# Kernel tuning notes

Hardware: AMD Instinct MI355X
Metric: run time of the kernel (lower is better)

## Reference

```python
import jax, jax.numpy as jnp
import numpy as np
import math

B, L, T, IN, H, DEPTH, HEADS = 4096, 1, 64, 16, 128, 3, 2
HD = H // HEADS
EPS = 1e-5


def layer_norm(x, g, b):
    u = jnp.mean(x, axis=-1, keepdims=True)
    s = jnp.mean((x - u) ** 2, axis=-1, keepdims=True)
    return g * (x - u) / jnp.sqrt(s + EPS) + b


def mlp(x, W, b, g, beta):
    return jax.nn.relu(layer_norm(x @ W + b, g, beta))


def attention(h, amask, Wq, bq, Wk, bk, Wv, bv):
    N, Tn, _ = h.shape
    def heads(x):
        return x.reshape(N, Tn, HEADS, HD).transpose(0, 2, 1, 3)
    q = heads(h @ Wq + bq)
    k = heads(h @ Wk + bk)
    v = heads(h @ Wv + bv)
    scores = jnp.einsum('nhqd,nhkd->nhqk', q, k) / math.sqrt(HD)
    scores = scores + (1.0 - amask[:, None]) * -10000.0
    probs = jax.nn.softmax(scores, axis=-1)
    ctx = jnp.einsum('nhqk,nhkd->nhqd', probs, v)
    return ctx.transpose(0, 2, 1, 3).reshape(N, Tn, H)


def setup_inputs() -> dict:
    key = jax.random.key(0)
    ks = jax.random.split(key, 8)
    feat = jax.random.normal(ks[0], (B, L, T, IN), jnp.float32)
    seq_lens = jax.random.randint(ks[1], (B, L), 1, T + 1)
    pos = jnp.arange(T)
    # repo convention: 0 = valid node, 1 = padded; prefix-valid layout
    masks = (pos[None, None, :] >= seq_lens[..., None]).astype(jnp.float32)[..., None]
    s = 0.02
    W_emb = jax.random.normal(ks[2], (IN, H), jnp.float32) * s
    W_enc = jax.random.normal(ks[3], (H, H), jnp.float32) * s
    Wq = jax.random.normal(ks[4], (DEPTH, H, H), jnp.float32) * s
    Wk = jax.random.normal(ks[5], (DEPTH, H, H), jnp.float32) * s
    Wv = jax.random.normal(ks[6], (DEPTH, H, H), jnp.float32) * s
    return dict(
        lane_nodes_feat=feat, masks=masks,
        W_emb=W_emb, b_emb=jnp.zeros((H,)), g_emb=jnp.ones((H,)), beta_emb=jnp.zeros((H,)),
        W_enc=W_enc, b_enc=jnp.zeros((H,)), g_enc=jnp.ones((H,)), beta_enc=jnp.zeros((H,)),
        Wq=Wq, bq=jnp.zeros((DEPTH, H)), Wk=Wk, bk=jnp.zeros((DEPTH, H)), Wv=Wv, bv=jnp.zeros((DEPTH, H)),
        ln_g=jnp.ones((DEPTH, H)), ln_b=jnp.zeros((DEPTH, H)),
    )


def reference(lane_nodes_feat, masks, W_emb, b_emb, g_emb, beta_emb, W_enc, b_enc,
              g_enc, beta_enc, Wq, bq, Wk, bk, Wv, bv, ln_g, ln_b):
    emb = mlp(lane_nodes_feat, W_emb, b_emb, g_emb, beta_emb)   # [B,L,T,H]
    emb = mlp(emb, W_enc, b_enc, g_enc, beta_enc)
    # every (b,l) lane has >=1 valid node by construction, so masked_select == reshape
    hs = emb.reshape(B * L, T, H)
    seq_lens = jnp.sum(1.0 - masks[:, :, :, 0], axis=-1).reshape(B * L)  # [N]
    pos = jnp.arange(T)
    valid = pos[None, :] < seq_lens[:, None]                              # [N,T]
    amask = (valid[:, :, None] & valid[:, None, :]).astype(hs.dtype)      # [N,T,T]
    for d in range(DEPTH):
        temp = hs
        hs = attention(hs, amask, Wq[d], bq[d], Wk[d], bk[d], Wv[d], bv[d])
        hs = jax.nn.relu(hs) + temp
        hs = layer_norm(hs, ln_g[d], ln_b[d])
    hs = jnp.max(hs, axis=1)                                              # [N,H]
    return hs.reshape(B, L, H)
```

## Files before the change

### kernel.cpp

```cpp
#include <hip/hip_runtime.h>

typedef unsigned short u16;
typedef unsigned int u32;
typedef __attribute__((ext_vector_type(8))) short short8;
typedef __attribute__((ext_vector_type(4))) float floatx4;

#define EPSV 1e-5f
#define WS_ELEMS 167936

__device__ __forceinline__ float b2f(u16 u){
  union { float f; u32 i; } c; c.i = ((u32)u) << 16; return c.f;
}
__device__ __forceinline__ u16 f2b(float f){
  union { float f; u32 i; } c; c.f = f;
  u32 r = c.i + 0x7FFFu + ((c.i >> 16) & 1u);
  return (u16)(r >> 16);
}
__device__ __forceinline__ u16 f2bc(float f){
  union { float f; u32 i; } c; c.f = f;
  return (u16)((c.i + 0x8000u) >> 16);
}
__device__ __forceinline__ float ldf(const void* p, int i, bool isf){
  return isf ? ((const float*)p)[i] : b2f(((const u16*)p)[i]);
}
__device__ __forceinline__ bool detect_f32(const void* g_emb){
  return *(const u32*)g_emb == 0x3F800000u;
}
__device__ __forceinline__ void dma16(const u16* g, u16* l){
  __builtin_amdgcn_global_load_lds((const __attribute__((address_space(1))) u32*)(g),
                                   (__attribute__((address_space(3))) u32*)(l), 16, 0, 0);
}
__device__ __forceinline__ void dma_slab(const u16* g, u16* dst, int wave, int lane){
  #pragma unroll
  for (int i = 0; i < 4; i++){
    int c = (wave << 2) + i;
    dma16(g + (c << 9) + (lane << 3), dst + (c << 9));
  }
}

__global__ void prep_kernel(const void* W_emb, const void* W_enc,
                            const void* Wq, const void* Wk, const void* Wv,
                            const void* g_emb, u16* ws){
  bool isf = detect_f32(g_emb);
  int e = blockIdx.x * 256 + threadIdx.x;
  if (e >= WS_ELEMS) return;
  float v;
  if (e < 4096){
    int half = e >> 11, r = e & 2047;
    int nt = r >> 9, q = (r >> 3) & 63, j = r & 7;
    int col = half*64 + nt*16 + (q & 15);
    int k = (q >> 4)*8 + j;
    v = (k < 16) ? ldf(W_emb, k*128 + col, isf) : 0.0f;
  } else if (e < 20480){
    int i = e - 4096;
    int half = i >> 13, r = i & 8191;
    int chunk = r >> 9, q = (r >> 3) & 63, j = r & 7;
    int ks = chunk >> 2, nt = chunk & 3;
    int col = half*64 + nt*16 + (q & 15);
    int k = ks*32 + (q >> 4)*8 + j;
    v = ldf(W_enc, k*128 + col, isf);
  } else {
    int i = e - 20480;
    int slab = i >> 13, r = i & 8191;
    int dh = slab / 3, which = slab - dh*3;
    int d = dh >> 1, h = dh & 1;
    int chunk = r >> 9, q = (r >> 3) & 63, j = r & 7;
    int ks = chunk >> 2, nt = chunk & 3;
    int col = h*64 + nt*16 + (q & 15);
    int k = ks*32 + (q >> 4)*8 + j;
    const void* W = (which == 0) ? Wv : (which == 1) ? Wk : Wq;
    v = ldf(W, d*16384 + k*128 + col, isf);
  }
  ws[e] = f2b(v);
}

__device__ __forceinline__ short8 frg(const u16* p, int chunk, int lane){
  return *(const short8*)(p + (chunk << 9) + (lane << 3));
}
__device__ __forceinline__ int wfoff(int wave, int nt, int lq, int lc){
  return ((((nt >> 1) << 2) + wave) << 9)
       + ((((((nt << 1) + (lc >> 3)) & 3) << 4) + (lq << 2)) << 3) + (lc & 7);
}
__device__ __forceinline__ int qfoff(int wave, int nt, int lq, int lc){
  return (wave << 10) + ((nt >> 1) << 9)
       + ((((((nt << 1) + (lc >> 3)) & 3) << 4) + (lq << 2)) << 3) + (lc & 7);
}

__device__ __forceinline__ void gemmW(const u16* sh, const u16* slab, int wave, int lane, floatx4* acc){
  #pragma unroll
  for (int ks = 0; ks < 4; ks++){
    short8 a = frg(sh, ks*4 + wave, lane);
    #pragma unroll
    for (int nt = 0; nt < 4; nt++)
      acc[nt] = __builtin_amdgcn_mfma_f32_16x16x32_bf16(a, frg(slab, ks*4 + nt, lane), acc[nt], 0, 0, 0);
  }
}
__device__ __forceinline__ void gemmWT(const u16* sh, const u16* slab, int wave, int lane, floatx4* acc){
  #pragma unroll
  for (int ks = 0; ks < 4; ks++){
    short8 a = frg(slab, ks*4 + wave, lane);
    #pragma unroll
    for (int nt = 0; nt < 4; nt++)
      acc[nt] = __builtin_amdgcn_mfma_f32_16x16x32_bf16(a, frg(sh, ks*4 + nt, lane), acc[nt], 0, 0, 0);
  }
}
__device__ __forceinline__ void gemm64(const u16* areg, const u16* b, int wave, int lane, floatx4* acc){
  #pragma unroll
  for (int ks = 0; ks < 2; ks++){
    short8 a = *(const short8*)(areg + (wave << 10) + (ks << 9) + (lane << 3));
    #pragma unroll
    for (int nt = 0; nt < 4; nt++)
      acc[nt] = __builtin_amdgcn_mfma_f32_16x16x32_bf16(a, frg(b, ks*4 + nt, lane), acc[nt], 0, 0, 0);
  }
}

__device__ __forceinline__ void red_sum2(float* s1, float* s2){
  #pragma unroll
  for (int m = 1; m < 16; m <<= 1){
    #pragma unroll
    for (int r = 0; r < 4; r++){
      s1[r] += __shfl_xor(s1[r], m, 64);
      s2[r] += __shfl_xor(s2[r], m, 64);
    }
  }
}

__device__ __forceinline__ void ln_mlp(floatx4* acc, const void* bias, const void* g,
    const void* bet, bool isf, int wave, int lq, int lc, u16* sh){
  float x[8][4], s1[4] = {0,0,0,0}, s2[4] = {0,0,0,0};
  #pragma unroll
  for (int nt = 0; nt < 8; nt++){
    float bb = ldf(bias, nt*16 + lc, isf);
    #pragma unroll
    for (int r = 0; r < 4; r++){
      float v = acc[nt][r] + bb;
      x[nt][r] = v; s1[r] += v; s2[r] += v*v;
    }
  }
  red_sum2(s1, s2);
  float mean[4], rstd[4];
  #pragma unroll
  for (int r = 0; r < 4; r++){
    mean[r] = s1[r] * (1.0f/128.0f);
    rstd[r] = rsqrtf(s2[r]*(1.0f/128.0f) - mean[r]*mean[r] + EPSV);
  }
  #pragma unroll
  for (int nt = 0; nt < 8; nt++){
    float gg = ldf(g, nt*16 + lc, isf), bb = ldf(bet, nt*16 + lc, isf);
    int o = wfoff(wave, nt, lq, lc);
    #pragma unroll
    for (int r = 0; r < 4; r++){
      float y = (x[nt][r] - mean[r]) * rstd[r] * gg + bb;
      sh[o + 8*r] = f2bc(fmaxf(y, 0.0f));
    }
  }
}

__device__ __forceinline__ void ln_attn(floatx4* ctx, const u16* cb,
                                        int wave, int lq, int lc, u16* sh){
  float x[8][4], s1[4] = {0,0,0,0}, s2[4] = {0,0,0,0};
  #pragma unroll
  for (int nt = 0; nt < 8; nt++){
    int o = wfoff(wave, nt, lq, lc);
    #pragma unroll
    for (int r = 0; r < 4; r++){
      float v = fmaxf(ctx[nt][r], 0.0f) + b2f(sh[o + 8*r]);
      x[nt][r] = v; s1[r] += v; s2[r] += v*v;
    }
  }
  red_sum2(s1, s2);
  float mean[4], rstd[4];
  #pragma unroll
  for (int r = 0; r < 4; r++){
    mean[r] = s1[r] * (1.0f/128.0f);
    rstd[r] = rsqrtf(s2[r]*(1.0f/128.0f) - mean[r]*mean[r] + EPSV);
  }
  #pragma unroll
  for (int nt = 0; nt < 8; nt++){
    float gg = b2f(cb[384 + nt*16 + lc]), bb = b2f(cb[512 + nt*16 + lc]);
    int o = wfoff(wave, nt, lq, lc);
    #pragma unroll
    for (int r = 0; r < 4; r++){
      float y = (x[nt][r] - mean[r]) * rstd[r] * gg + bb;
      sh[o + 8*r] = f2bc(y);
    }
  }
}

__global__ __launch_bounds__(256, 3)
void fused_kernel(const void* feat, const void* masks,
                  const void* b_emb, const void* g_emb, const void* be_emb,
                  const void* b_enc, const void* g_enc, const void* be_enc,
                  const void* bq, const void* bk, const void* bv,
                  const void* ln_g, const void* ln_b,
                  const u16* ws, void* out){
  __shared__ __align__(16) u16 s_h[8192];
  __shared__ __align__(16) u16 s_w[8192];
  __shared__ __align__(16) u16 s_k[4096];
  __shared__ __align__(16) u16 s_v[4096];
  __shared__ u16 s_c[1920];
  __shared__ float s_valid[64];

  int tid = threadIdx.x;
  int wave = tid >> 6, lane = tid & 63, lq = lane >> 4, lc = lane & 15;
  int n = blockIdx.x;
  bool isf = detect_f32(g_emb);
  const floatx4 z4 = {0.0f, 0.0f, 0.0f, 0.0f};

  dma16(ws + ((wave*2 + 0) << 9) + (lane << 3), s_w + ((wave*2 + 0) << 9));
  dma16(ws + ((wave*2 + 1) << 9) + (lane << 3), s_w + ((wave*2 + 1) << 9));

  if (!isf){
    const u16* fp = (const u16*)feat + n*1024;
    if (tid < 128){
      int t = tid >> 1, half = tid & 1;
      uint4 v = *(const uint4*)(fp + t*16 + half*8);
      *(uint4*)(s_h + ((t >> 4) << 9) + (((half << 4) + (t & 15)) << 3)) = v;
    } else {
      int t = (tid - 128) >> 1, half = 2 + ((tid - 128) & 1);
      uint4 z; z.x = z.y = z.z = z.w = 0;
      *(uint4*)(s_h + ((t >> 4) << 9) + (((half << 4) + (t & 15)) << 3)) = z;
    }
  } else {
    for (int i = tid; i < 2048; i += 256){
      int t = i >> 5, k = i & 31;
      float v = (k < 16) ? ((const float*)feat)[n*1024 + t*16 + k] : 0.0f;
      s_h[((t >> 4) << 9) + ((((k >> 3) << 4) + (t & 15)) << 3) + (k & 7)] = f2b(v);
    }
  }
  for (int i = tid; i < 1920; i += 256){
    int blk = i >> 7, off = i & 127;
    int d = blk / 5, wh = blk - d*5;
    const void* src = (wh == 0) ? bq : (wh == 1) ? bk : (wh == 2) ? bv : (wh == 3) ? ln_g : ln_b;
    s_c[i] = isf ? f2b(((const float*)src)[d*128 + off]) : ((const u16*)src)[d*128 + off];
  }
  if (tid < 64) s_valid[tid] = (ldf(masks, n*64 + tid, isf) == 0.0f) ? 1.0f : 0.0f;
  __syncthreads();

  floatx4 acc[8];
  #pragma unroll
  for (int i = 0; i < 8; i++) acc[i] = z4;
  {
    short8 a = frg(s_h, wave, lane);
    #pragma unroll
    for (int nt = 0; nt < 4; nt++){
      acc[nt]     = __builtin_amdgcn_mfma_f32_16x16x32_bf16(a, frg(s_w, nt,     lane), acc[nt],     0,0,0);
      acc[4 + nt] = __builtin_amdgcn_mfma_f32_16x16x32_bf16(a, frg(s_w, 4 + nt, lane), acc[4 + nt], 0,0,0);
    }
  }
  __syncthreads();
  dma_slab(ws + 4096, s_w, wave, lane);
  ln_mlp(acc, b_emb, g_emb, be_emb, isf, wave, lq, lc, s_h);
  __syncthreads();

  #pragma unroll
  for (int i = 0; i < 8; i++) acc[i] = z4;
  gemmW(s_h, s_w, wave, lane, acc);
  __syncthreads();
  dma_slab(ws + 12288, s_w, wave, lane);
  __syncthreads();
  gemmW(s_h, s_w, wave, lane, acc + 4);
  __syncthreads();
  dma_slab(ws + 20480, s_w, wave, lane);
  ln_mlp(acc, b_enc, g_enc, be_enc, isf, wave, lq, lc, s_h);
  __syncthreads();

  int sb = 20480;
  for (int d = 0; d < 3; d++){
    const u16* cb = s_c + d*640;
    floatx4 ctx[8];
    #pragma unroll
    for (int i = 0; i < 8; i++) ctx[i] = z4;

    for (int h = 0; h < 2; h++){
      floatx4 pa[4];
      #pragma unroll
      for (int i = 0; i < 4; i++) pa[i] = z4;
      gemmWT(s_h, s_w, wave, lane, pa);
      __syncthreads();
      dma_slab(ws + sb + 8192, s_w, wave, lane);
      {
        float bb4[4];
        #pragma unroll
        for (int r = 0; r < 4; r++) bb4[r] = b2f(cb[256 + h*64 + wave*16 + (lq << 2) + r]);
        #pragma unroll
        for (int nt = 0; nt < 4; nt++){
          int o = wfoff(wave, nt, lq, lc);
          #pragma unroll
          for (int r = 0; r < 4; r++) s_v[o + 8*r] = f2bc(pa[nt][r] + bb4[r]);
        }
      }
      __syncthreads();
      #pragma unroll
      for (int i = 0; i < 4; i++) pa[i] = z4;
      gemmW(s_h, s_w, wave, lane, pa);
      __syncthreads();
      dma_slab(ws + sb + 16384, s_w, wave, lane);
      {
        #pragma unroll
        for (int nt = 0; nt < 4; nt++){
          float bb = b2f(cb[128 + h*64 + nt*16 + lc]);
          int o = wfoff(wave, nt, lq, lc);
          #pragma unroll
          for (int r = 0; r < 4; r++) s_k[o + 8*r] = f2bc(pa[nt][r] + bb);
        }
      }
      __syncthreads();
      #pragma unroll
      for (int i = 0; i < 4; i++) pa[i] = z4;
      gemmW(s_h, s_w, wave, lane, pa);
      __syncthreads();
      {
        #pragma unroll
        for (int nt = 0; nt < 4; nt++){
          float bb = b2f(cb[h*64 + nt*16 + lc]);
          int o = qfoff(wave, nt, lq, lc);
          #pragma unroll
          for (int r = 0; r < 4; r++) s_w[o + 8*r] = f2bc(pa[nt][r] + bb);
        }
      }
      #pragma unroll
      for (int i = 0; i < 4; i++) pa[i] = z4;
      gemm64(s_w, s_k, wave, lane, pa);

      float rv[4], cv[4];
      #pragma unroll
      for (int r = 0; r < 4; r++) rv[r] = s_valid[wave*16 + (lq << 2) + r];
      #pragma unroll
      for (int nt = 0; nt < 4; nt++) cv[nt] = s_valid[nt*16 + lc];

      float p[4][4];
      #pragma unroll
      for (int nt = 0; nt < 4; nt++)
        #pragma unroll
        for (int r = 0; r < 4; r++)
          p[nt][r] = pa[nt][r]*0.125f - 10000.0f*(1.0f - rv[r]*cv[nt]);

      float mx[4];
      #pragma unroll
      for (int r = 0; r < 4; r++)
        mx[r] = fmaxf(fmaxf(p[0][r], p[1][r]), fmaxf(p[2][r], p[3][r]));
      #pragma unroll
      for (int m = 1; m < 16; m <<= 1)
        #pragma unroll
        for (int r = 0; r < 4; r++) mx[r] = fmaxf(mx[r], __shfl_xor(mx[r], m, 64));

      float sm[4] = {0,0,0,0};
      #pragma unroll
      for (int nt = 0; nt < 4; nt++)
        #pragma unroll
        for (int r = 0; r < 4; r++){ p[nt][r] = __expf(p[nt][r] - mx[r]); sm[r] += p[nt][r]; }
      #pragma unroll
      for (int m = 1; m < 16; m <<= 1)
        #pragma unroll
        for (int r = 0; r < 4; r++) sm[r] += __shfl_xor(sm[r], m, 64);

      float inv[4];
      #pragma unroll
      for (int r = 0; r < 4; r++) inv[r] = 1.0f / sm[r];

      #pragma unroll
      for (int nt = 0; nt < 4; nt++){
        int o = qfoff(wave, nt, lq, lc);
        #pragma unroll
        for (int r = 0; r < 4; r++) s_w[o + 8*r] = f2bc(p[nt][r] * inv[r]);
      }
      gemm64(s_w, s_v, wave, lane, ctx + h*4);
      __syncthreads();
      sb += 24576;
      if (!(d == 2 && h == 1)) dma_slab(ws + sb, s_w, wave, lane);
      if (h == 1) ln_attn(ctx, cb, wave, lq, lc, s_h);
      __syncthreads();
    }
  }

  if (tid < 128){
    int col = tid;
    float mxv = -1e30f;
    #pragma unroll 4
    for (int t = 0; t < 64; t++)
      mxv = fmaxf(mxv, b2f(s_h[((((col >> 5) << 2) + (t >> 4)) << 9)
                               + (((((col >> 3) & 3) << 4) + (t & 15)) << 3) + (col & 7)]));
    if (isf) ((float*)out)[n*128 + col] = mxv;
    else     ((u16*)out)[n*128 + col] = f2b(mxv);
  }
}

extern "C" void kernel_launch(void* const* d_in, const int* in_sizes, int n_in,
                              void* d_out, int out_size, void* d_ws, size_t ws_size,
                              hipStream_t stream){
  const void* feat   = d_in[0];
  const void* masks  = d_in[1];
  const void* W_emb  = d_in[2];
  const void* b_emb  = d_in[3];
  const void* g_emb  = d_in[4];
  const void* be_emb = d_in[5];
  const void* W_enc  = d_in[6];
  const void* b_enc  = d_in[7];
  const void* g_enc  = d_in[8];
  const void* be_enc = d_in[9];
  const void* Wq     = d_in[10];
  const void* bq     = d_in[11];
  const void* Wk     = d_in[12];
  const void* bk     = d_in[13];
  const void* Wv     = d_in[14];
  const void* bv     = d_in[15];
  const void* ln_g   = d_in[16];
  const void* ln_b   = d_in[17];
  u16* ws = (u16*)d_ws;

  hipLaunchKernelGGL(prep_kernel, dim3((WS_ELEMS + 255)/256), dim3(256), 0, stream,
                     W_emb, W_enc, Wq, Wk, Wv, g_emb, ws);
  hipLaunchKernelGGL(fused_kernel, dim3(4096), dim3(256), 0, stream,
                     feat, masks, b_emb, g_emb, be_emb, b_enc, g_enc, be_enc,
                     bq, bk, bv, ln_g, ln_b, ws, d_out);
}
```

Baseline: 389.9 us.

## Swizzle LDS fragment layout, 2x2 wave tiling for QKV GEMMs, keep residual in registers

Introduces an XOR-swizzled fragment layout for LDS tiles and prepacked weights to reduce bank conflicts on fragment reads and writes. The per-head Q/K/V projections switch from a 1x4 per-wave tiling to a 2x2 wave tiling, so each wave loads fewer distinct fragments per k-step. The residual activations are kept in fp32 registers (xres) rather than re-read from LDS as bf16, which removes LDS reads and rounding of the residual at the cost of 32 extra registers per thread, a risk at 3 blocks per CU.

```diff
diff --git a/kernel.cpp b/kernel.cpp
--- a/kernel.cpp
+++ b/kernel.cpp
@@ -36,6 +36,15 @@
     int c = (wave << 2) + i;
     dma16(g + (c << 9) + (lane << 3), dst + (c << 9));
   }
+}
+__device__ __forceinline__ int swz(int lane){
+  return (lane & ~3) | ((lane ^ (lane >> 2)) & 3);
+}
+__device__ __forceinline__ int fragoff(int chunk, int quad, int m, int j){
+  return (chunk << 9) + ((((quad << 4) | (m & 12) | ((m ^ (m >> 2)) & 3))) << 3) + j;
+}
+__device__ __forceinline__ short8 frg(const u16* p, int chunk, int swl){
+  return *(const short8*)(p + (chunk << 9) + (swl << 3));
 }
 
 __global__ void prep_kernel(const void* W_emb, const void* W_enc,
@@ -47,17 +56,19 @@
   float v;
   if (e < 4096){
     int half = e >> 11, r = e & 2047;
-    int nt = r >> 9, q = (r >> 3) & 63, j = r & 7;
-    int col = half*64 + nt*16 + (q & 15);
-    int k = (q >> 4)*8 + j;
+    int q = (r >> 3) & 63, j = r & 7;
+    int ql = (q & ~3) | ((q ^ (q >> 2)) & 3);
+    int col = half*64 + ((r >> 9) << 4) + (ql & 15);
+    int k = (ql >> 4)*8 + j;
     v = (k < 16) ? ldf(W_emb, k*128 + col, isf) : 0.0f;
   } else if (e < 20480){
     int i = e - 4096;
     int half = i >> 13, r = i & 8191;
     int chunk = r >> 9, q = (r >> 3) & 63, j = r & 7;
+    int ql = (q & ~3) | ((q ^ (q >> 2)) & 3);
     int ks = chunk >> 2, nt = chunk & 3;
-    int col = half*64 + nt*16 + (q & 15);
-    int k = ks*32 + (q >> 4)*8 + j;
+    int col = half*64 + nt*16 + (ql & 15);
+    int k = ks*32 + (ql >> 4)*8 + j;
     v = ldf(W_enc, k*128 + col, isf);
   } else {
     int i = e - 20480;
@@ -65,52 +76,38 @@
     int dh = slab / 3, which = slab - dh*3;
     int d = dh >> 1, h = dh & 1;
     int chunk = r >> 9, q = (r >> 3) & 63, j = r & 7;
+    int ql = (q & ~3) | ((q ^ (q >> 2)) & 3);
     int ks = chunk >> 2, nt = chunk & 3;
-    int col = h*64 + nt*16 + (q & 15);
-    int k = ks*32 + (q >> 4)*8 + j;
+    int col = h*64 + nt*16 + (ql & 15);
+    int k = ks*32 + (ql >> 4)*8 + j;
     const void* W = (which == 0) ? Wv : (which == 1) ? Wk : Wq;
     v = ldf(W, d*16384 + k*128 + col, isf);
   }
   ws[e] = f2b(v);
 }
 
-__device__ __forceinline__ short8 frg(const u16* p, int chunk, int lane){
-  return *(const short8*)(p + (chunk << 9) + (lane << 3));
-}
-__device__ __forceinline__ int wfoff(int wave, int nt, int lq, int lc){
-  return ((((nt >> 1) << 2) + wave) << 9)
-       + ((((((nt << 1) + (lc >> 3)) & 3) << 4) + (lq << 2)) << 3) + (lc & 7);
-}
-__device__ __forceinline__ int qfoff(int wave, int nt, int lq, int lc){
-  return (wave << 10) + ((nt >> 1) << 9)
-       + ((((((nt << 1) + (lc >> 3)) & 3) << 4) + (lq << 2)) << 3) + (lc & 7);
-}
-
-__device__ __forceinline__ void gemmW(const u16* sh, const u16* slab, int wave, int lane, floatx4* acc){
+#define MFMA(a,b,c) __builtin_amdgcn_mfma_f32_16x16x32_bf16((a),(b),(c),0,0,0)
+
+__device__ __forceinline__ void gemmW(const u16* sh, const u16* slab, int wave, int swl, floatx4* acc){
   #pragma unroll
   for (int ks = 0; ks < 4; ks++){
-    short8 a = frg(sh, ks*4 + wave, lane);
+    short8 a = frg(sh, ks*4 + wave, swl);
     #pragma unroll
     for (int nt = 0; nt < 4; nt++)
-      acc[nt] = __builtin_amdgcn_mfma_f32_16x16x32_bf16(a, frg(slab, ks*4 + nt, lane), acc[nt], 0, 0, 0);
-  }
-}
-__device__ __forceinline__ void gemmWT(const u16* sh, const u16* slab, int wave, int lane, floatx4* acc){
+      acc[nt] = MFMA(a, frg(slab, ks*4 + nt, swl), acc[nt]);
+  }
+}
+__device__ __forceinline__ void gemm2x2(const u16* A, const u16* B, int ra, int cb_, int swl, floatx4* acc){
   #pragma unroll
   for (int ks = 0; ks < 4; ks++){
-    short8 a = frg(slab, ks*4 + wave, lane);
-    #pragma unroll
-    for (int nt = 0; nt < 4; nt++)
-      acc[nt] = __builtin_amdgcn_mfma_f32_16x16x32_bf16(a, frg(sh, ks*4 + nt, lane), acc[nt], 0, 0, 0);
-  }
-}
-__device__ __forceinline__ void gemm64(const u16* areg, const u16* b, int wave, int lane, floatx4* acc){
-  #pragma unroll
-  for (int ks = 0; ks < 2; ks++){
-    short8 a = *(const short8*)(areg + (wave << 10) + (ks << 9) + (lane << 3));
-    #pragma unroll
-    for (int nt = 0; nt < 4; nt++)
-      acc[nt] = __builtin_amdgcn_mfma_f32_16x16x32_bf16(a, frg(b, ks*4 + nt, lane), acc[nt], 0, 0, 0);
+    short8 a0 = frg(A, ks*4 + ra,     swl);
+    short8 a1 = frg(A, ks*4 + ra + 1, swl);
+    short8 b0 = frg(B, ks*4 + cb_,     swl);
+    short8 b1 = frg(B, ks*4 + cb_ + 1, swl);
+    acc[0] = MFMA(a0, b0, acc[0]);
+    acc[1] = MFMA(a0, b1, acc[1]);
+    acc[2] = MFMA(a1, b0, acc[2]);
+    acc[3] = MFMA(a1, b1, acc[3]);
   }
 }
 
@@ -125,16 +122,46 @@
   }
 }
 
+__device__ __forceinline__ void pwrite_col(floatx4* a4, u16* dst, const u16* bias,
+    int wr, int wc, int lq, int lc){
+  #pragma unroll
+  for (int tc = 0; tc < 2; tc++){
+    float bb = b2f(bias[wc*32 + tc*16 + lc]);
+    #pragma unroll
+    for (int tr = 0; tr < 2; tr++){
+      #pragma unroll
+      for (int r = 0; r < 4; r++)
+        dst[fragoff(wc*4 + wr*2 + tr, tc*2 + (lc >> 3), lq*4 + r, lc & 7)]
+          = f2bc(a4[tr*2+tc][r] + bb);
+    }
+  }
+}
+__device__ __forceinline__ void pwrite_row(floatx4* a4, u16* dst, const u16* bias,
+    int wr, int wc, int lq, int lc){
+  #pragma unroll
+  for (int tr = 0; tr < 2; tr++){
+    float bb[4];
+    #pragma unroll
+    for (int r = 0; r < 4; r++) bb[r] = b2f(bias[wr*32 + tr*16 + lq*4 + r]);
+    #pragma unroll
+    for (int tc = 0; tc < 2; tc++)
+      #pragma unroll
+      for (int r = 0; r < 4; r++)
+        dst[fragoff(wc*4 + wr*2 + tr, tc*2 + (lc >> 3), lq*4 + r, lc & 7)]
+          = f2bc(a4[tr*2+tc][r] + bb[r]);
+  }
+}
+
 __device__ __forceinline__ void ln_mlp(floatx4* acc, const void* bias, const void* g,
-    const void* bet, bool isf, int wave, int lq, int lc, u16* sh){
-  float x[8][4], s1[4] = {0,0,0,0}, s2[4] = {0,0,0,0};
+    const void* bet, bool isf, float xres[8][4], int wave, int lq, int lc, u16* sh){
+  float s1[4] = {0,0,0,0}, s2[4] = {0,0,0,0};
   #pragma unroll
   for (int nt = 0; nt < 8; nt++){
     float bb = ldf(bias, nt*16 + lc, isf);
     #pragma unroll
     for (int r = 0; r < 4; r++){
       float v = acc[nt][r] + bb;
-      x[nt][r] = v; s1[r] += v; s2[r] += v*v;
+      xres[nt][r] = v; s1[r] += v; s2[r] += v*v;
     }
   }
   red_sum2(s1, s2);
@@ -147,27 +174,25 @@
   #pragma unroll
   for (int nt = 0; nt < 8; nt++){
     float gg = ldf(g, nt*16 + lc, isf), bb = ldf(bet, nt*16 + lc, isf);
-    int o = wfoff(wave, nt, lq, lc);
     #pragma unroll
     for (int r = 0; r < 4; r++){
-      float y = (x[nt][r] - mean[r]) * rstd[r] * gg + bb;
-      sh[o + 8*r] = f2bc(fmaxf(y, 0.0f));
-    }
-  }
-}
-
-__device__ __forceinline__ void ln_attn(floatx4* ctx, const u16* cb,
+      float y = fmaxf((xres[nt][r] - mean[r]) * rstd[r] * gg + bb, 0.0f);
+      xres[nt][r] = y;
+      sh[fragoff((nt >> 1)*4 + wave, ((nt & 1) << 1) + (lc >> 3), lq*4 + r, lc & 7)] = f2bc(y);
+    }
+  }
+}
+
+__device__ __forceinline__ void ln_attn(floatx4* ctx, float xres[8][4], const u16* cb,
                                         int wave, int lq, int lc, u16* sh){
-  float x[8][4], s1[4] = {0,0,0,0}, s2[4] = {0,0,0,0};
-  #pragma unroll
-  for (int nt = 0; nt < 8; nt++){
-    int o = wfoff(wave, nt, lq, lc);
+  float s1[4] = {0,0,0,0}, s2[4] = {0,0,0,0};
+  #pragma unroll
+  for (int nt = 0; nt < 8; nt++)
     #pragma unroll
     for (int r = 0; r < 4; r++){
-      float v = fmaxf(ctx[nt][r], 0.0f) + b2f(sh[o + 8*r]);
-      x[nt][r] = v; s1[r] += v; s2[r] += v*v;
-    }
-  }
+      float v = fmaxf(ctx[nt][r], 0.0f) + xres[nt][r];
+      xres[nt][r] = v; s1[r] += v; s2[r] += v*v;
+    }
   red_sum2(s1, s2);
   float mean[4], rstd[4];
   #pragma unroll
@@ -178,11 +203,11 @@
   #pragma unroll
   for (int nt = 0; nt < 8; nt++){
     float gg = b2f(cb[384 + nt*16 + lc]), bb = b2f(cb[512 + nt*16 + lc]);
-    int o = wfoff(wave, nt, lq, lc);
     #pragma unroll
     for (int r = 0; r < 4; r++){
-      float y = (x[nt][r] - mean[r]) * rstd[r] * gg + bb;
-      sh[o + 8*r] = f2bc(y);
+      float y = (xres[nt][r] - mean[r]) * rstd[r] * gg + bb;
+      xres[nt][r] = y;
+      sh[fragoff((nt >> 1)*4 + wave, ((nt & 1) << 1) + (lc >> 3), lq*4 + r, lc & 7)] = f2bc(y);
     }
   }
 }
@@ -203,6 +228,8 @@
 
   int tid = threadIdx.x;
   int wave = tid >> 6, lane = tid & 63, lq = lane >> 4, lc = lane & 15;
+  int wr = wave >> 1, wc = wave & 1;
+  int swl = swz(lane);
   int n = blockIdx.x;
   bool isf = detect_f32(g_emb);
   const floatx4 z4 = {0.0f, 0.0f, 0.0f, 0.0f};
@@ -215,17 +242,17 @@
     if (tid < 128){
       int t = tid >> 1, half = tid & 1;
       uint4 v = *(const uint4*)(fp + t*16 + half*8);
-      *(uint4*)(s_h + ((t >> 4) << 9) + (((half << 4) + (t & 15)) << 3)) = v;
+      *(uint4*)(s_h + fragoff(t >> 4, half, t & 15, 0)) = v;
     } else {
       int t = (tid - 128) >> 1, half = 2 + ((tid - 128) & 1);
       uint4 z; z.x = z.y = z.z = z.w = 0;
-      *(uint4*)(s_h + ((t >> 4) << 9) + (((half << 4) + (t & 15)) << 3)) = z;
+      *(uint4*)(s_h + fragoff(t >> 4, half, t & 15, 0)) = z;
     }
   } else {
     for (int i = tid; i < 2048; i += 256){
       int t = i >> 5, k = i & 31;
       float v = (k < 16) ? ((const float*)feat)[n*1024 + t*16 + k] : 0.0f;
-      s_h[((t >> 4) << 9) + ((((k >> 3) << 4) + (t & 15)) << 3) + (k & 7)] = f2b(v);
+      s_h[fragoff(t >> 4, k >> 3, t & 15, k & 7)] = f2b(v);
     }
   }
   for (int i = tid; i < 1920; i += 256){
@@ -237,32 +264,33 @@
   if (tid < 64) s_valid[tid] = (ldf(masks, n*64 + tid, isf) == 0.0f) ? 1.0f : 0.0f;
   __syncthreads();
 
+  float xres[8][4];
   floatx4 acc[8];
   #pragma unroll
   for (int i = 0; i < 8; i++) acc[i] = z4;
   {
-    short8 a = frg(s_h, wave, lane);
+    short8 a = frg(s_h, wave, swl);
     #pragma unroll
     for (int nt = 0; nt < 4; nt++){
-      acc[nt]     = __builtin_amdgcn_mfma_f32_16x16x32_bf16(a, frg(s_w, nt,     lane), acc[nt],     0,0,0);
-      acc[4 + nt] = __builtin_amdgcn_mfma_f32_16x16x32_bf16(a, frg(s_w, 4 + nt, lane), acc[4 + nt], 0,0,0);
+      acc[nt]     = MFMA(a, frg(s_w, nt,     swl), acc[nt]);
+      acc[4 + nt] = MFMA(a, frg(s_w, 4 + nt, swl), acc[4 + nt]);
     }
   }
   __syncthreads();
   dma_slab(ws + 4096, s_w, wave, lane);
-  ln_mlp(acc, b_emb, g_emb, be_emb, isf, wave, lq, lc, s_h);
+  ln_mlp(acc, b_emb, g_emb, be_emb, isf, xres, wave, lq, lc, s_h);
   __syncthreads();
 
   #pragma unroll
   for (int i = 0; i < 8; i++) acc[i] = z4;
-  gemmW(s_h, s_w, wave, lane, acc);
+  gemmW(s_h, s_w, wave, swl, acc);
   __syncthreads();
   dma_slab(ws + 12288, s_w, wave, lane);
   __syncthreads();
-  gemmW(s_h, s_w, wave, lane, acc + 4);
+  gemmW(s_h, s_w, wave, swl, acc + 4);
   __syncthreads();
   dma_slab(ws + 20480, s_w, wave, lane);
-  ln_mlp(acc, b_enc, g_enc, be_enc, isf, wave, lq, lc, s_h);
+  ln_mlp(acc, b_enc, g_enc, be_enc, isf, xres, wave, lq, lc, s_h);
   __syncthreads();
 
   int sb = 20480;
@@ -276,53 +304,33 @@
       floatx4 pa[4];
       #pragma unroll
       for (int i = 0; i < 4; i++) pa[i] = z4;
-      gemmWT(s_h, s_w, wave, lane, pa);
+      gemm2x2(s_w, s_h, wr*2, wc*2, swl, pa);
       __syncthreads();
       dma_slab(ws + sb + 8192, s_w, wave, lane);
-      {
-        float bb4[4];
-        #pragma unroll
-        for (int r = 0; r < 4; r++) bb4[r] = b2f(cb[256 + h*64 + wave*16 + (lq << 2) + r]);
-        #pragma unroll
-        for (int nt = 0; nt < 4; nt++){
-          int o = wfoff(wave, nt, lq, lc);
-          #pragma unroll
-          for (int r = 0; r < 4; r++) s_v[o + 8*r] = f2bc(pa[nt][r] + bb4[r]);
-        }
+      pwrite_row(pa, s_v, cb + 256 + h*64, wr, wc, lq, lc);
+      __syncthreads();
+      #pragma unroll
+      for (int i = 0; i < 4; i++) pa[i] = z4;
+      gemm2x2(s_h, s_w, wr*2, wc*2, swl, pa);
+      __syncthreads();
+      dma_slab(ws + sb + 16384, s_w, wave, lane);
+      pwrite_col(pa, s_k, cb + 128 + h*64, wr, wc, lq, lc);
+      __syncthreads();
+      #pragma unroll
+      for (int i = 0; i < 4; i++) pa[i] = z4;
+      gemm2x2(s_h, s_w, wr*2, wc*2, swl, pa);
+      __syncthreads();
+      pwrite_col(pa, s_w, cb + h*64, wr, wc, lq, lc);
+      __syncthreads();
+      #pragma unroll
+      for (int i = 0; i < 4; i++) pa[i] = z4;
+      #pragma unroll
+      for (int ks = 0; ks < 2; ks++){
+        short8 a = frg(s_w, ks*4 + wave, swl);
+        #pragma unroll
+        for (int nt = 0; nt < 4; nt++)
+          pa[nt] = MFMA(a, frg(s_k, ks*4 + nt, swl), pa[nt]);
       }
-      __syncthreads();
-      #pragma unroll
-      for (int i = 0; i < 4; i++) pa[i] = z4;
-      gemmW(s_h, s_w, wave, lane, pa);
-      __syncthreads();
-      dma_slab(ws + sb + 16384, s_w, wave, lane);
-      {
-        #pragma unroll
-        for (int nt = 0; nt < 4; nt++){
-          float bb = b2f(cb[128 + h*64 + nt*16 + lc]);
-          int o = wfoff(wave, nt, lq, lc);
-          #pragma unroll
-          for (int r = 0; r < 4; r++) s_k[o + 8*r] = f2bc(pa[nt][r] + bb);
-        }
-      }
-      __syncthreads();
-      #pragma unroll
-      for (int i = 0; i < 4; i++) pa[i] = z4;
-      gemmW(s_h, s_w, wave, lane, pa);
-      __syncthreads();
-      {
-        #pragma unroll
-        for (int nt = 0; nt < 4; nt++){
-          float bb = b2f(cb[h*64 + nt*16 + lc]);
-          int o = qfoff(wave, nt, lq, lc);
-          #pragma unroll
-          for (int r = 0; r < 4; r++) s_w[o + 8*r] = f2bc(pa[nt][r] + bb);
-        }
-      }
-      #pragma unroll
-      for (int i = 0; i < 4; i++) pa[i] = z4;
-      gemm64(s_w, s_k, wave, lane, pa);
-
       float rv[4], cv[4];
       #pragma unroll
       for (int r = 0; r < 4; r++) rv[r] = s_valid[wave*16 + (lq << 2) + r];
@@ -360,16 +368,22 @@
       for (int r = 0; r < 4; r++) inv[r] = 1.0f / sm[r];
 
       #pragma unroll
-      for (int nt = 0; nt < 4; nt++){
-        int o = qfoff(wave, nt, lq, lc);
-        #pragma unroll
-        for (int r = 0; r < 4; r++) s_w[o + 8*r] = f2bc(p[nt][r] * inv[r]);
+      for (int nt = 0; nt < 4; nt++)
+        #pragma unroll
+        for (int r = 0; r < 4; r++)
+          s_w[fragoff(8 + 2*wave + (nt >> 1), ((nt & 1) << 1) + (lc >> 3), lq*4 + r, lc & 7)]
+            = f2bc(p[nt][r] * inv[r]);
+      #pragma unroll
+      for (int ks = 0; ks < 2; ks++){
+        short8 a = frg(s_w, 8 + 2*wave + ks, swl);
+        #pragma unroll
+        for (int nt = 0; nt < 4; nt++)
+          ctx[h*4 + nt] = MFMA(a, frg(s_v, ks*4 + nt, swl), ctx[h*4 + nt]);
       }
-      gemm64(s_w, s_v, wave, lane, ctx + h*4);
       __syncthreads();
       sb += 24576;
       if (!(d == 2 && h == 1)) dma_slab(ws + sb, s_w, wave, lane);
-      if (h == 1) ln_attn(ctx, cb, wave, lq, lc, s_h);
+      if (h == 1) ln_attn(ctx, xres, cb, wave, lq, lc, s_h);
       __syncthreads();
     }
   }
@@ -379,8 +393,7 @@
     float mxv = -1e30f;
     #pragma unroll 4
     for (int t = 0; t < 64; t++)
-      mxv = fmaxf(mxv, b2f(s_h[((((col >> 5) << 2) + (t >> 4)) << 9)
-                               + (((((col >> 3) & 3) << 4) + (t & 15)) << 3) + (col & 7)]));
+      mxv = fmaxf(mxv, b2f(s_h[fragoff(((col >> 5) << 2) + (t >> 4), (col >> 3) & 3, t & 15, col & 7)]));
     if (isf) ((float*)out)[n*128 + col] = mxv;
     else     ((u16*)out)[n*128 + col] = f2b(mxv);
   }
```

Result: slower. 399.3 us (+2.4%).
